# Kernel optimization log

Measured on AMD Instinct MI355X. Metric: run time of the kernel, lower is better.

The kernel has to match this reference:

```python
import jax, jax.numpy as jnp
import numpy as np

N_EMBD = 1024
N_HEAD = 16
B, T = 2, 2048


def setup_inputs() -> dict:
    key = jax.random.key(0)
    k1, k2, k3 = jax.random.split(key, 3)
    scale = 1.0 / np.sqrt(N_EMBD)
    x = jax.random.normal(k1, (B, T, N_EMBD), dtype=jnp.float32)
    W_qkv = jax.random.normal(k2, (N_EMBD, 3 * N_EMBD), dtype=jnp.float32) * scale
    b_qkv = jnp.zeros((3 * N_EMBD,), dtype=jnp.float32)
    W_proj = jax.random.normal(k3, (N_EMBD, N_EMBD), dtype=jnp.float32) * scale
    b_proj = jnp.zeros((N_EMBD,), dtype=jnp.float32)
    return {"x": x, "W_qkv": W_qkv, "b_qkv": b_qkv, "W_proj": W_proj, "b_proj": b_proj}


def reference(x, W_qkv, b_qkv, W_proj, b_proj):
    Bx, Tx, C = x.shape
    H = N_HEAD
    D = C // H  # head_size
    qkv = x @ W_qkv + b_qkv  # [B,T,3C]
    Q, K, V = jnp.split(qkv, 3, axis=2)
    # [B,T,C] -> [B,H,T,D]
    Q = Q.reshape(Bx, Tx, H, D).transpose(0, 2, 1, 3)
    K = K.reshape(Bx, Tx, H, D).transpose(0, 2, 1, 3)
    V = V.reshape(Bx, Tx, H, D).transpose(0, 2, 1, 3)
    scores = jnp.einsum("bhqd,bhkd->bhqk", Q, K) / jnp.sqrt(jnp.float32(D))
    causal = jnp.tril(jnp.ones((Tx, Tx), dtype=bool))
    scores = jnp.where(causal, scores, jnp.float32(-jnp.inf))
    weights = jax.nn.softmax(scores, axis=-1)
    out = jnp.einsum("bhqk,bhkd->bhqd", weights, V)  # [B,H,T,D]
    out = out.transpose(0, 2, 1, 3).reshape(Bx, Tx, C)
    return out @ W_proj + b_proj
```

## Files before the change

### kernel.cpp

```cpp
#include <hip/hip_runtime.h>
#include <hip/hip_bf16.h>
#include <math.h>

#define BB 2
#define TT 2048
#define CC 1024
#define HH 16
#define DD 64
#define C3 3072
#define BT 4096

typedef __attribute__((ext_vector_type(8))) short short8;
typedef __attribute__((ext_vector_type(8))) unsigned short ushort8;
typedef __attribute__((ext_vector_type(4))) unsigned short ushort4v;
typedef __attribute__((ext_vector_type(4))) float floatx4;

__device__ __forceinline__ unsigned short f2b(float f) {
    union { float f; unsigned int u; } v; v.f = f;
    unsigned int u = v.u;
    unsigned int r = (u + 0x7fffu + ((u >> 16) & 1u)) >> 16;
    return (unsigned short)r;
}
__device__ __forceinline__ unsigned short f2b_fast(float f) {
    unsigned int u = __builtin_bit_cast(unsigned int, f);
    return (unsigned short)((u + 0x8000u) >> 16);
}

__device__ __forceinline__ void store_out(unsigned short* p, float v) { *p = f2b(v); }
__device__ __forceinline__ void store_out(float* p, float v) { *p = v; }

__device__ __forceinline__ void async16(const unsigned short* g, unsigned short* lds) {
    __builtin_amdgcn_global_load_lds(
        (const __attribute__((address_space(1))) unsigned int*)g,
        (__attribute__((address_space(3))) unsigned int*)lds, 16, 0, 0);
}

__global__ __launch_bounds__(256) void cast_kernel(
    const float* __restrict__ in, unsigned short* __restrict__ out, int n8)
{
    int i = blockIdx.x * 256 + threadIdx.x;
    if (i >= n8) return;
    const float4 v0 = *(const float4*)&in[(size_t)i * 8];
    const float4 v1 = *(const float4*)&in[(size_t)i * 8 + 4];
    ushort8 pk;
    pk[0] = f2b(v0.x); pk[1] = f2b(v0.y); pk[2] = f2b(v0.z); pk[3] = f2b(v0.w);
    pk[4] = f2b(v1.x); pk[5] = f2b(v1.y); pk[6] = f2b(v1.z); pk[7] = f2b(v1.w);
    *(ushort8*)&out[(size_t)i * 8] = pk;
}

__global__ __launch_bounds__(256) void transpose_cast2_kernel(
    const float* __restrict__ Wqkv, const float* __restrict__ Wproj,
    unsigned short* __restrict__ Wqkv_t, unsigned short* __restrict__ Wproj_t)
{
    __shared__ float tile[64 * 65];
    const int tid = threadIdx.x;
    const int xt = blockIdx.x;
    const float* src; unsigned short* dst; int Ccols, c0;
    if (xt < 48) { src = Wqkv;  dst = Wqkv_t;  Ccols = C3; c0 = xt * 64; }
    else         { src = Wproj; dst = Wproj_t; Ccols = CC; c0 = (xt - 48) * 64; }
    const int r0 = blockIdx.y * 64;
#pragma unroll
    for (int it = 0; it < 4; it++) {
        int idx = it * 256 + tid;
        int row = idx >> 4;
        int c4  = idx & 15;
        float4 v = *(const float4*)&src[(size_t)(r0 + row) * Ccols + c0 + c4 * 4];
        tile[row * 65 + c4 * 4 + 0] = v.x;
        tile[row * 65 + c4 * 4 + 1] = v.y;
        tile[row * 65 + c4 * 4 + 2] = v.z;
        tile[row * 65 + c4 * 4 + 3] = v.w;
    }
    __syncthreads();
#pragma unroll
    for (int it = 0; it < 2; it++) {
        int idx = it * 256 + tid;
        int orow = idx >> 3;
        int o8   = idx & 7;
        ushort8 pk;
#pragma unroll
        for (int j = 0; j < 8; j++) pk[j] = f2b(tile[(o8 * 8 + j) * 65 + orow]);
        *(ushort8*)&dst[(size_t)(c0 + orow) * CC + r0 + o8 * 8] = pk;
    }
}

template <typename OUT_T, bool WVT>
__global__ __launch_bounds__(256) void gemm_bt_kernel(
    const unsigned short* __restrict__ A, const unsigned short* __restrict__ Bm,
    const float* __restrict__ bias, OUT_T* __restrict__ Cmat,
    unsigned short* __restrict__ Vt,
    int M, int N, int K, float qscale, int qcols)
{
    __shared__ __align__(16) unsigned short sA[128 * 64];
    __shared__ __align__(16) unsigned short sB[128 * 64];

    const int tid = threadIdx.x;
    const int lane16 = tid & 15, quad = (tid & 63) >> 4;
    const int w = tid >> 6;
    const int wm = w >> 1, wn = w & 1;
    const int m0 = blockIdx.y * 128, n0 = blockIdx.x * 128;
    const int lx = lane16 & 7;

    floatx4 acc[4][4] = {};

    for (int kt = 0; kt < K; kt += 64) {
#pragma unroll
        for (int it = 0; it < 4; it++) {
            int idx = it * 256 + tid;
            int row = idx >> 3;
            int c8m = (idx & 7) ^ (row & 7);
            int wslot = it * 256 + (tid & 192);
            async16(&A[(size_t)(m0 + row) * K + kt + c8m * 8], &sA[wslot * 8]);
            async16(&Bm[(size_t)(n0 + row) * K + kt + c8m * 8], &sB[wslot * 8]);
        }
        __syncthreads();
#pragma unroll
        for (int ks = 0; ks < 64; ks += 32) {
            const int slot = ((ks >> 3) + quad) ^ lx;
            short8 af[4], bf[4];
#pragma unroll
            for (int t = 0; t < 4; t++) {
                af[t] = *(const short8*)&sA[(wm * 64 + t * 16 + lane16) * 64 + slot * 8];
                bf[t] = *(const short8*)&sB[(wn * 64 + t * 16 + lane16) * 64 + slot * 8];
            }
#pragma unroll
            for (int mt = 0; mt < 4; mt++)
#pragma unroll
                for (int nt = 0; nt < 4; nt++)
                    acc[mt][nt] = __builtin_amdgcn_mfma_f32_16x16x32_bf16(
                        af[mt], bf[nt], acc[mt][nt], 0, 0, 0);
        }
        __syncthreads();
    }

#pragma unroll
    for (int mt = 0; mt < 4; mt++) {
#pragma unroll
        for (int nt = 0; nt < 4; nt++) {
            int col = n0 + wn * 64 + nt * 16 + lane16;
            float bv = bias[col];
            float sc = (col < qcols) ? qscale : 1.0f;
            float v[4];
            int row0 = m0 + wm * 64 + mt * 16 + quad * 4;
#pragma unroll
            for (int r = 0; r < 4; r++) {
                v[r] = (acc[mt][nt][r] + bv) * sc;
                store_out(&Cmat[(size_t)(row0 + r) * N + col], v[r]);
            }
            if (WVT && n0 >= 2 * CC) {
                int hd = col - 2 * CC;
                int b  = row0 >> 11;
                int token = row0 & (TT - 1);
                ushort4v pk;
#pragma unroll
                for (int r = 0; r < 4; r++) pk[r] = f2b(v[r]);
                *(ushort4v*)&Vt[((size_t)(b * HH * DD) + hd) * TT + token] = pk;
            }
        }
    }
}

__global__ __launch_bounds__(256) void attn_mfma_kernel(
    const unsigned short* __restrict__ qkv, const unsigned short* __restrict__ Vt,
    unsigned short* __restrict__ att)
{
    __shared__ __align__(16) unsigned short Ks[64 * 72];
    __shared__ __align__(16) unsigned short Vs[64 * 72];
    __shared__ __align__(16) unsigned short Pl[64 * 76];

    const int tid = threadIdx.x;
    const int l = tid & 63;
    const int lane16 = l & 15, quad = l >> 4;
    const int w = tid >> 6;
    const int bh = blockIdx.y;
    const int b = bh >> 4, h = bh & 15;
    const int g = blockIdx.x;

    const int srow = tid >> 3;
    const int sc8  = (tid & 7) * 8;
    const unsigned short* kbase = &qkv[(size_t)(b * TT) * C3 + CC + h * DD + sc8];
    const unsigned short* vbase = &Vt[(size_t)(bh * DD + srow) * TT + sc8];

#pragma unroll
    for (int pass = 0; pass < 2; ++pass) {
        const int p  = pass ? g : (31 - g);
        const int q0 = p * 64;
        const int qw = q0 + w * 16;

        short8 qf[2];
        {
            const unsigned short* qp =
                &qkv[(size_t)(b * TT + qw + lane16) * C3 + h * DD + quad * 8];
            qf[0] = *(const short8*)&qp[0];
            qf[1] = *(const short8*)&qp[32];
        }

        float psum[4] = {0.f, 0.f, 0.f, 0.f};
        floatx4 O[4] = {};

        ushort8 kr0 = *(const ushort8*)&kbase[(size_t)srow * C3];
        ushort8 kr1 = *(const ushort8*)&kbase[(size_t)(srow + 32) * C3];
        ushort8 vr0 = *(const ushort8*)&vbase[0];
        ushort8 vr1 = *(const ushort8*)&vbase[(size_t)32 * TT];

        const int ntiles = p + 1;
        for (int t = 0; t < ntiles; ++t) {
            const int k0 = t * 64;
            __syncthreads();
            *(ushort8*)&Ks[srow * 72 + sc8]        = kr0;
            *(ushort8*)&Ks[(srow + 32) * 72 + sc8] = kr1;
            *(ushort8*)&Vs[srow * 72 + sc8]        = vr0;
            *(ushort8*)&Vs[(srow + 32) * 72 + sc8] = vr1;
            __syncthreads();

            if (t + 1 < ntiles) {
                const int kn = k0 + 64;
                kr0 = *(const ushort8*)&kbase[(size_t)(kn + srow) * C3];
                kr1 = *(const ushort8*)&kbase[(size_t)(kn + srow + 32) * C3];
                vr0 = *(const ushort8*)&vbase[kn];
                vr1 = *(const ushort8*)&vbase[(size_t)32 * TT + kn];
            }

            floatx4 s4[4] = {};
#pragma unroll
            for (int nt = 0; nt < 4; nt++) {
                short8 kf0 = *(const short8*)&Ks[(nt * 16 + lane16) * 72 + quad * 8];
                short8 kf1 = *(const short8*)&Ks[(nt * 16 + lane16) * 72 + 32 + quad * 8];
                s4[nt] = __builtin_amdgcn_mfma_f32_16x16x32_bf16(qf[0], kf0, s4[nt], 0, 0, 0);
                s4[nt] = __builtin_amdgcn_mfma_f32_16x16x32_bf16(qf[1], kf1, s4[nt], 0, 0, 0);
            }

            const bool diag = (t == ntiles - 1);
#pragma unroll
            for (int nt = 0; nt < 4; nt++) {
                int key = k0 + nt * 16 + lane16;
#pragma unroll
                for (int r = 0; r < 4; r++) {
                    float v = s4[nt][r];
                    if (diag) v = (key > qw + quad * 4 + r) ? -1e30f : v;
                    float pe = __expf(v);
                    psum[r] += pe;
                    Pl[(w * 16 + quad * 4 + r) * 76 + nt * 16 + lane16] = f2b_fast(pe);
                }
            }
            __threadfence_block();

            short8 pf0 = *(const short8*)&Pl[(w * 16 + lane16) * 76 + quad * 8];
            short8 pf1 = *(const short8*)&Pl[(w * 16 + lane16) * 76 + 32 + quad * 8];
#pragma unroll
            for (int dt = 0; dt < 4; dt++) {
                short8 vf0 = *(const short8*)&Vs[(dt * 16 + lane16) * 72 + quad * 8];
                short8 vf1 = *(const short8*)&Vs[(dt * 16 + lane16) * 72 + 32 + quad * 8];
                O[dt] = __builtin_amdgcn_mfma_f32_16x16x32_bf16(pf0, vf0, O[dt], 0, 0, 0);
                O[dt] = __builtin_amdgcn_mfma_f32_16x16x32_bf16(pf1, vf1, O[dt], 0, 0, 0);
            }
        }

#pragma unroll
        for (int off = 1; off <= 8; off <<= 1)
#pragma unroll
            for (int r = 0; r < 4; r++)
                psum[r] += __shfl_xor(psum[r], off, 64);

        float rl[4];
#pragma unroll
        for (int r = 0; r < 4; r++) rl[r] = 1.0f / psum[r];
#pragma unroll
        for (int dt = 0; dt < 4; dt++)
#pragma unroll
            for (int r = 0; r < 4; r++) {
                int qq = qw + quad * 4 + r;
                int d = dt * 16 + lane16;
                att[(size_t)(b * TT + qq) * CC + h * DD + d] = f2b(O[dt][r] * rl[r]);
            }
    }
}

extern "C" void kernel_launch(void* const* d_in, const int* in_sizes, int n_in,
                              void* d_out, int out_size, void* d_ws, size_t ws_size,
                              hipStream_t stream) {
    const float* x     = (const float*)d_in[0];
    const float* Wqkv  = (const float*)d_in[1];
    const float* bqkv  = (const float*)d_in[2];
    const float* Wproj = (const float*)d_in[3];
    const float* bproj = (const float*)d_in[4];
    float* out = (float*)d_out;

    unsigned short* xb      = (unsigned short*)d_ws;
    unsigned short* qkv_b   = xb      + (size_t)BT * CC;
    unsigned short* Wqkv_t  = qkv_b   + (size_t)BT * C3;
    unsigned short* Wproj_t = Wqkv_t  + (size_t)C3 * CC;
    unsigned short* Vt      = Wproj_t + (size_t)CC * CC;
    unsigned short* att_b   = Vt      + (size_t)BB * HH * DD * TT;

    cast_kernel<<<BT * CC / 8 / 256, 256, 0, stream>>>(x, xb, BT * CC / 8);
    {
        dim3 g(64, 16);
        transpose_cast2_kernel<<<g, 256, 0, stream>>>(Wqkv, Wproj, Wqkv_t, Wproj_t);
    }
    {
        dim3 grid(C3 / 128, BT / 128);
        gemm_bt_kernel<unsigned short, true><<<grid, 256, 0, stream>>>(
            xb, Wqkv_t, bqkv, qkv_b, Vt, BT, C3, CC, 0.125f, CC);
    }
    {
        dim3 grid(16, BB * HH);
        attn_mfma_kernel<<<grid, 256, 0, stream>>>(qkv_b, Vt, att_b);
    }
    {
        dim3 grid(CC / 128, BT / 128);
        gemm_bt_kernel<float, false><<<grid, 256, 0, stream>>>(
            att_b, Wproj_t, bproj, out, nullptr, BT, CC, CC, 1.0f, 0);
    }
}
```

Baseline: 186.7 us.

## Merge prep kernels, fold log2e into Q scale, swap attention grid axes

Fuses the x cast and the weight transpose-cast into one prep kernel, removing a launch. Folds log2(e) into the Q scaling in the QKV GEMM so attention can use exp2f instead of __expf. Swaps the attention grid so consecutive blocks cover different heads rather than different query groups, which changes scheduling order and cache locality. The exp2 change relies on the scale fold keeping softmax equivalent.

```diff
diff --git a/kernel.cpp b/kernel.cpp
--- a/kernel.cpp
+++ b/kernel.cpp
@@ -35,30 +35,32 @@
         (__attribute__((address_space(3))) unsigned int*)lds, 16, 0, 0);
 }
 
-__global__ __launch_bounds__(256) void cast_kernel(
-    const float* __restrict__ in, unsigned short* __restrict__ out, int n8)
-{
-    int i = blockIdx.x * 256 + threadIdx.x;
-    if (i >= n8) return;
-    const float4 v0 = *(const float4*)&in[(size_t)i * 8];
-    const float4 v1 = *(const float4*)&in[(size_t)i * 8 + 4];
-    ushort8 pk;
-    pk[0] = f2b(v0.x); pk[1] = f2b(v0.y); pk[2] = f2b(v0.z); pk[3] = f2b(v0.w);
-    pk[4] = f2b(v1.x); pk[5] = f2b(v1.y); pk[6] = f2b(v1.z); pk[7] = f2b(v1.w);
-    *(ushort8*)&out[(size_t)i * 8] = pk;
-}
-
-__global__ __launch_bounds__(256) void transpose_cast2_kernel(
+__global__ __launch_bounds__(256) void prep_kernel(
+    const float* __restrict__ x, unsigned short* __restrict__ xb,
     const float* __restrict__ Wqkv, const float* __restrict__ Wproj,
     unsigned short* __restrict__ Wqkv_t, unsigned short* __restrict__ Wproj_t)
 {
     __shared__ float tile[64 * 65];
     const int tid = threadIdx.x;
-    const int xt = blockIdx.x;
+    const int bid = blockIdx.x;
+
+    if (bid < 2048) {
+        int i = bid * 256 + tid;
+        const float4 v0 = *(const float4*)&x[(size_t)i * 8];
+        const float4 v1 = *(const float4*)&x[(size_t)i * 8 + 4];
+        ushort8 pk;
+        pk[0] = f2b(v0.x); pk[1] = f2b(v0.y); pk[2] = f2b(v0.z); pk[3] = f2b(v0.w);
+        pk[4] = f2b(v1.x); pk[5] = f2b(v1.y); pk[6] = f2b(v1.z); pk[7] = f2b(v1.w);
+        *(ushort8*)&xb[(size_t)i * 8] = pk;
+        return;
+    }
+
+    const int xt = bid - 2048;
+    const int cxt = xt & 63;
+    const int r0  = (xt >> 6) * 64;
     const float* src; unsigned short* dst; int Ccols, c0;
-    if (xt < 48) { src = Wqkv;  dst = Wqkv_t;  Ccols = C3; c0 = xt * 64; }
-    else         { src = Wproj; dst = Wproj_t; Ccols = CC; c0 = (xt - 48) * 64; }
-    const int r0 = blockIdx.y * 64;
+    if (cxt < 48) { src = Wqkv;  dst = Wqkv_t;  Ccols = C3; c0 = cxt * 64; }
+    else          { src = Wproj; dst = Wproj_t; Ccols = CC; c0 = (cxt - 48) * 64; }
 #pragma unroll
     for (int it = 0; it < 4; it++) {
         int idx = it * 256 + tid;
@@ -171,9 +173,9 @@
     const int l = tid & 63;
     const int lane16 = l & 15, quad = l >> 4;
     const int w = tid >> 6;
-    const int bh = blockIdx.y;
+    const int bh = blockIdx.x;
     const int b = bh >> 4, h = bh & 15;
-    const int g = blockIdx.x;
+    const int g = blockIdx.y;
 
     const int srow = tid >> 3;
     const int sc8  = (tid & 7) * 8;
@@ -237,7 +239,7 @@
                 for (int r = 0; r < 4; r++) {
                     float v = s4[nt][r];
                     if (diag) v = (key > qw + quad * 4 + r) ? -1e30f : v;
-                    float pe = __expf(v);
+                    float pe = exp2f(v);
                     psum[r] += pe;
                     Pl[(w * 16 + quad * 4 + r) * 76 + nt * 16 + lane16] = f2b_fast(pe);
                 }
@@ -292,18 +294,15 @@
     unsigned short* Vt      = Wproj_t + (size_t)CC * CC;
     unsigned short* att_b   = Vt      + (size_t)BB * HH * DD * TT;
 
-    cast_kernel<<<BT * CC / 8 / 256, 256, 0, stream>>>(x, xb, BT * CC / 8);
-    {
-        dim3 g(64, 16);
-        transpose_cast2_kernel<<<g, 256, 0, stream>>>(Wqkv, Wproj, Wqkv_t, Wproj_t);
-    }
+    prep_kernel<<<3072, 256, 0, stream>>>(x, xb, Wqkv, Wproj, Wqkv_t, Wproj_t);
+
     {
         dim3 grid(C3 / 128, BT / 128);
         gemm_bt_kernel<unsigned short, true><<<grid, 256, 0, stream>>>(
-            xb, Wqkv_t, bqkv, qkv_b, Vt, BT, C3, CC, 0.125f, CC);
+            xb, Wqkv_t, bqkv, qkv_b, Vt, BT, C3, CC, 0.125f * 1.44269504f, CC);
     }
     {
-        dim3 grid(16, BB * HH);
+        dim3 grid(BB * HH, 16);
         attn_mfma_kernel<<<grid, 256, 0, stream>>>(qkv_b, Vt, att_b);
     }
     {
```

Result: no change. 185.9 us (-0.4%).
